# Optimization experiments

Hardware: AMD Instinct MI355X
Metric: run time of the kernel (lower is better)

## Reference

```python
import jax, jax.numpy as jnp
import numpy as np

TRUNCATE = 4.0
SIGMA_MIN, SIGMA_MAX, NUM_STEPS = 0.5, 20.0, 200
RADIUS = int(TRUNCATE * SIGMA_MAX + 0.5)  # 80
KSIZE = 2 * RADIUS + 1                    # 161
B, C, H, W = 64, 3, 512, 512


def setup_inputs() -> dict:
    key = jax.random.key(0)
    k1, k2 = jax.random.split(key)
    x = jax.random.normal(k1, (B, C, H, W), dtype=jnp.float32)
    # geometric sigma schedule, as used in inverse-heat-dissipation models
    blur_sigmas = jnp.exp(
        jnp.linspace(np.log(SIGMA_MIN), np.log(SIGMA_MAX), NUM_STEPS)
    ).astype(jnp.float32)
    fwd_steps = jax.random.randint(k2, (B,), 0, NUM_STEPS, dtype=jnp.int32)
    return {"x": x, "blur_sigmas": blur_sigmas, "fwd_steps": fwd_steps}


def _gaussian_kernels_1d(sigmas, dtype):
    # torchvision formula: normalized exp(-0.5*(t/sigma)^2) on linspace(-half, half, K)
    half = (KSIZE - 1) / 2.0
    t = jnp.linspace(-half, half, KSIZE, dtype=dtype)        # [K]
    pdf = jnp.exp(-0.5 * (t[None, :] / sigmas[:, None]) ** 2)  # [B, K]
    return pdf / pdf.sum(axis=1, keepdims=True)


def reference(x, blur_sigmas, fwd_steps):
    b, c, h, w = x.shape
    sig = blur_sigmas[fwd_steps] + 1e-6                      # [B] per-sample sigma
    k1d = _gaussian_kernels_1d(sig, x.dtype)                 # [B, K]
    kc = jnp.repeat(k1d, c, axis=0)                          # [B*C, K] depthwise

    pad = KSIZE // 2
    xp = jnp.pad(x, ((0, 0), (0, 0), (pad, pad), (pad, pad)), mode="reflect")
    lhs = xp.reshape(1, b * c, h + 2 * pad, w + 2 * pad)

    dn_shape = (1, b * c, 1, 1)  # placeholder rhs shape for dim numbers
    dn = jax.lax.conv_dimension_numbers(lhs.shape, (b * c, 1, KSIZE, 1),
                                        ("NCHW", "OIHW", "NCHW"))
    # vertical pass: [1, BC, H+2p, W+2p] -> [1, BC, H, W+2p]
    y = jax.lax.conv_general_dilated(
        lhs, kc.reshape(b * c, 1, KSIZE, 1), (1, 1), "VALID",
        dimension_numbers=dn, feature_group_count=b * c)
    # horizontal pass: -> [1, BC, H, W]
    y = jax.lax.conv_general_dilated(
        y, kc.reshape(b * c, 1, 1, KSIZE), (1, 1), "VALID",
        dimension_numbers=dn, feature_group_count=b * c)
    return y.reshape(b, c, h, w)
```

## Files before the change

### kernel.cpp

```cpp
#include <hip/hip_runtime.h>
#include <hip/hip_fp16.h>


#define B_   64
#define C_   3
#define H_   512
#define W_   512
#define RMAX 80
#define NW   224
#define WOFF 112
#define RROW1 416
#define IW2   672

typedef float    f32x16 __attribute__((ext_vector_type(16)));
typedef _Float16 f16x8  __attribute__((ext_vector_type(8)));

__device__ __forceinline__ int refl(int g) {
    int a = g < 0 ? -g : g;
    int c = 1022 - a;
    return a < c ? a : c;
}

__device__ __forceinline__ int make_weights(float sigma, float* scr, float* red,
                                            unsigned int* w2v, int tid) {
    const int d = tid - 128;
    float e = 0.f;
    if (d >= -RMAX && d <= RMAX) {
        const float u = (float)d / sigma;
        e = expf(-0.5f * u * u);
    }
    scr[tid] = e;
    red[tid] = e;
    __syncthreads();
    for (int s = 128; s > 0; s >>= 1) {
        if (tid < s) red[tid] += red[tid + s];
        __syncthreads();
    }
    const float inv = 1.0f / red[0];
    int r = (int)ceilf(6.0f * sigma);
    if (r > RMAX) r = RMAX;
    if (r < 1)    r = 1;
    if (tid < NW) {
        const int d0 = tid - 112;
        const float w0 = (d0     >= -r && d0     <= r) ? scr[tid + 16] * inv : 0.f;
        const float w1 = (d0 + 1 >= -r && d0 + 1 <= r) ? scr[tid + 17] * inv : 0.f;
        w2v[tid] = (unsigned int)__half_as_ushort(__float2half(w0)) |
                   ((unsigned int)__half_as_ushort(__float2half(w1)) << 16);
    }
    __syncthreads();
    return r;
}

__global__ __launch_bounds__(256) void k_pass1(const float* __restrict__ x,
                                               const float* __restrict__ sig,
                                               const int* __restrict__ steps,
                                               __half* __restrict__ tmp) {
    __shared__ __align__(16) unsigned short sh[64 * RROW1];
    __shared__ unsigned int w2v[NW];
    const int tid = threadIdx.x;
    int bid = blockIdx.x;
    bid = ((bid & 7) * 384) + (bid >> 3);
    const int bc  = bid >> 4;
    const int rem = bid & 15;
    const int y0  = (rem >> 3) << 8;
    const int x0  = (rem & 7) << 6;
    const int b   = bc / C_;
    const size_t img = (size_t)bc * (H_ * (size_t)W_);

    const float sigma = sig[steps[b]] + 1e-6f;
    float* scr = (float*)sh;
    const int r  = make_weights(sigma, scr, scr + 256, w2v, tid);
    const int rp = (r + 7) & ~7;
    const int ns = (r + rp + 47) >> 4;
    const int Rr = 224 + 16 * ns;
    const int ystart = y0 - rp;

    {
        const int p0 = tid & 15;
        const int x4 = tid >> 4;
        const float* gsrc = x + img + (size_t)(x0 + x4 * 4);
        const int i7 = (2 * p0) & 7;
        for (int pr = p0; 2 * pr < Rr; pr += 16) {
            const int i0  = 2 * pr;
            const int gy0 = refl(ystart + i0);
            const int gy1 = refl(ystart + i0 + 1);
            const float4 va = *(const float4*)(gsrc + (size_t)gy0 * W_);
            const float4 vb = *(const float4*)(gsrc + (size_t)gy1 * W_);
            const float* fa = (const float*)&va;
            const float* fb = (const float*)&vb;
            const int c = i0 >> 3;
            #pragma unroll
            for (int q = 0; q < 4; ++q) {
                const int xq = x4 * 4 + q;
                const int hidx = xq * RROW1 + ((c ^ (xq & 3)) << 3) + i7;
                *(__half2*)(sh + hidx) = __floats2half2_rn(fa[q], fb[q]);
            }
        }
    }
    __syncthreads();

    const int l   = tid & 63;
    const int wv_ = tid >> 6;
    const int m   = l & 31;
    const int g   = l >> 5;
    const int key = m & 3;
    const int ebase = WOFF + 8 * g - rp - m;
    const int cA  = 4 * wv_ + g;
    const int cB  = 4 * (wv_ + 4) + g;
    const unsigned short* shm0 = sh + m * RROW1;
    const unsigned short* shm1 = sh + (32 + m) * RROW1;

    f32x16 a0 = {}, a1 = {}, a2 = {}, a3 = {};
    for (int s = 0; s < ns; ++s) {
        const int e = ebase + 16 * s;
        union { unsigned int u[4]; f16x8 h; } A;
        A.u[0] = w2v[e];     A.u[1] = w2v[e + 2];
        A.u[2] = w2v[e + 4]; A.u[3] = w2v[e + 6];
        const int phA = ((cA + 2 * s) ^ key) << 3;
        const int phB = ((cB + 2 * s) ^ key) << 3;
        const f16x8 b00 = *(const f16x8*)(shm0 + phA);
        const f16x8 b01 = *(const f16x8*)(shm1 + phA);
        const f16x8 b10 = *(const f16x8*)(shm0 + phB);
        const f16x8 b11 = *(const f16x8*)(shm1 + phB);
        a0 = __builtin_amdgcn_mfma_f32_32x32x16_f16(A.h, b00, a0, 0, 0, 0);
        a1 = __builtin_amdgcn_mfma_f32_32x32x16_f16(A.h, b01, a1, 0, 0, 0);
        a2 = __builtin_amdgcn_mfma_f32_32x32x16_f16(A.h, b10, a2, 0, 0, 0);
        a3 = __builtin_amdgcn_mfma_f32_32x32x16_f16(A.h, b11, a3, 0, 0, 0);
    }

    __half* tb0 = tmp + img + (size_t)(y0 + 32 * wv_) * W_ + x0 + m;
    __half* tb1 = tmp + img + (size_t)(y0 + 32 * (wv_ + 4)) * W_ + x0 + m;
    #pragma unroll
    for (int reg = 0; reg < 16; ++reg) {
        const int row = (reg & 3) + 8 * (reg >> 2) + 4 * g;
        tb0[(size_t)row * W_]      = __float2half(a0[reg]);
        tb0[(size_t)row * W_ + 32] = __float2half(a1[reg]);
        tb1[(size_t)row * W_]      = __float2half(a2[reg]);
        tb1[(size_t)row * W_ + 32] = __float2half(a3[reg]);
    }
}

__global__ __launch_bounds__(256) void k_pass2(const __half* __restrict__ tmp,
                                               const float* __restrict__ sig,
                                               const int* __restrict__ steps,
                                               float* __restrict__ out) {
    __shared__ __align__(16) unsigned short sh[32 * IW2];
    __shared__ unsigned int w2v[NW];
    const int tid = threadIdx.x;
    const int bid = blockIdx.x;
    const int bc  = bid >> 4;
    const int y0  = (bid & 15) << 5;
    const int b   = bc / C_;
    const size_t img = (size_t)bc * (H_ * (size_t)W_);

    const float sigma = sig[steps[b]] + 1e-6f;
    float* scr = (float*)sh;
    const int r  = make_weights(sigma, scr, scr + 256, w2v, tid);
    const int rp = (r + 7) & ~7;
    const int ns = (r + rp + 47) >> 4;

    const int row  = tid >> 3;
    const int cq   = tid & 7;
    const int rkey = row & 3;
    {
        const __half* grow = tmp + img + (size_t)(y0 + row) * W_;
        const int cb = rp >> 3;
        for (int k = cq; k < 64; k += 8) {
            const int c = cb + k;
            *(int4*)(sh + row * IW2 + ((c ^ rkey) << 3)) =
                *(const int4*)(grow + k * 8);
        }
    }
    __syncthreads();
    {
        const int nh = 16 * ns - 32;
        const int rbase = row * IW2;
        for (int e = cq; e < nh; e += 8) {
            const int ip = e < rp ? e : e + 512;
            const int gx = ip - rp;
            const int is = refl(gx) + rp;
            const unsigned short v =
                sh[rbase + (((is >> 3) ^ rkey) << 3) + (is & 7)];
            sh[rbase + (((ip >> 3) ^ rkey) << 3) + (ip & 7)] = v;
        }
    }
    __syncthreads();

    const int l   = tid & 63;
    const int wv_ = tid >> 6;
    const int m   = l & 31;
    const int g   = l >> 5;
    const int akey  = m & 3;
    const int ebase = WOFF + 8 * g - rp - m;
    const unsigned short* shm = sh + m * IW2;
    const int c0 = 16 * wv_ + g;

    f32x16 a0 = {}, a1 = {}, a2 = {}, a3 = {};
    for (int s = 0; s < ns; ++s) {
        const int e = ebase + 16 * s;
        union { unsigned int u[4]; f16x8 h; } Wf;
        Wf.u[0] = w2v[e];     Wf.u[1] = w2v[e + 2];
        Wf.u[2] = w2v[e + 4]; Wf.u[3] = w2v[e + 6];
        const int cs = c0 + 2 * s;
        const f16x8 f0 = *(const f16x8*)(shm + (((cs     ) ^ akey) << 3));
        const f16x8 f1 = *(const f16x8*)(shm + (((cs +  4) ^ akey) << 3));
        const f16x8 f2 = *(const f16x8*)(shm + (((cs +  8) ^ akey) << 3));
        const f16x8 f3 = *(const f16x8*)(shm + (((cs + 12) ^ akey) << 3));
        a0 = __builtin_amdgcn_mfma_f32_32x32x16_f16(f0, Wf.h, a0, 0, 0, 0);
        a1 = __builtin_amdgcn_mfma_f32_32x32x16_f16(f1, Wf.h, a1, 0, 0, 0);
        a2 = __builtin_amdgcn_mfma_f32_32x32x16_f16(f2, Wf.h, a2, 0, 0, 0);
        a3 = __builtin_amdgcn_mfma_f32_32x32x16_f16(f3, Wf.h, a3, 0, 0, 0);
    }

    float* ob = out + img + (size_t)y0 * W_ + 128 * wv_ + m;
    #pragma unroll
    for (int reg = 0; reg < 16; ++reg) {
        const int orow = (reg & 3) + 8 * (reg >> 2) + 4 * g;
        float* orp_ = ob + (size_t)orow * W_;
        orp_[0]  = a0[reg];
        orp_[32] = a1[reg];
        orp_[64] = a2[reg];
        orp_[96] = a3[reg];
    }
}

extern "C" void kernel_launch(void* const* d_in, const int* in_sizes, int n_in,
                              void* d_out, int out_size, void* d_ws, size_t ws_size,
                              hipStream_t stream) {
    const float* x     = (const float*)d_in[0];
    const float* sig   = (const float*)d_in[1];
    const int*   steps = (const int*)d_in[2];
    float* out = (float*)d_out;
    __half* tmp = (__half*)d_ws;

    k_pass1<<<B_ * C_ * 16, 256, 0, stream>>>(x, sig, steps, tmp);
    k_pass2<<<B_ * C_ * 16, 256, 0, stream>>>(tmp, sig, steps, out);
}
```

Measured before the change: 398.3 us.

## Fuse vertical and horizontal blur passes into one kernel via LDS intermediate

Merges the two separable-convolution kernels into one. Each block computes the vertical pass for a 32-row strip in eight 64-column chunks and keeps the fp16 result in LDS, then runs the horizontal pass from LDS. This removes the fp16 intermediate round-trip through global memory and one kernel launch. In exchange, each block re-reads the vertical halo rows (up to 2*r extra input rows per 32 output rows), and only two of four waves do MFMA work during the vertical stage, with syncthreads between chunks.

After: 478.5 us. 1.2x slower.

```diff
diff --git a/kernel.cpp b/kernel.cpp
--- a/kernel.cpp
+++ b/kernel.cpp
@@ -9,8 +9,8 @@
 #define RMAX 80
 #define NW   224
 #define WOFF 112
-#define RROW1 416
-#define IW2   672
+#define SB_R 192
+#define IW   704
 
 typedef float    f32x16 __attribute__((ext_vector_type(16)));
 typedef _Float16 f16x8  __attribute__((ext_vector_type(8)));
@@ -51,157 +51,109 @@
     return r;
 }
 
-__global__ __launch_bounds__(256) void k_pass1(const float* __restrict__ x,
-                                               const float* __restrict__ sig,
-                                               const int* __restrict__ steps,
-                                               __half* __restrict__ tmp) {
-    __shared__ __align__(16) unsigned short sh[64 * RROW1];
+__global__ __launch_bounds__(256, 2) void k_fused(const float* __restrict__ x,
+                                                  const float* __restrict__ sig,
+                                                  const int* __restrict__ steps,
+                                                  float* __restrict__ out) {
+    __shared__ __align__(16) unsigned short sbuf[64 * SB_R];
+    __shared__ __align__(16) unsigned short vtmp[32 * IW];
     __shared__ unsigned int w2v[NW];
     const int tid = threadIdx.x;
-    int bid = blockIdx.x;
-    bid = ((bid & 7) * 384) + (bid >> 3);
-    const int bc  = bid >> 4;
-    const int rem = bid & 15;
-    const int y0  = (rem >> 3) << 8;
-    const int x0  = (rem & 7) << 6;
+    const int id  = blockIdx.x;
+    const int xcd = id & 7, idx = id >> 3;
+    const int bc  = xcd * 24 + (idx >> 4);
+    const int y0  = (idx & 15) << 5;
     const int b   = bc / C_;
     const size_t img = (size_t)bc * (H_ * (size_t)W_);
 
     const float sigma = sig[steps[b]] + 1e-6f;
-    float* scr = (float*)sh;
+    float* scr = (float*)sbuf;
     const int r  = make_weights(sigma, scr, scr + 256, w2v, tid);
     const int rp = (r + 7) & ~7;
     const int ns = (r + rp + 47) >> 4;
-    const int Rr = 224 + 16 * ns;
+    const int Rr = 16 * ns;
     const int ystart = y0 - rp;
 
+    const int l  = tid & 63;
+    const int wv = tid >> 6;
+    const int m  = l & 31;
+    const int g  = l >> 5;
+    const int ebase = WOFF + 8 * g - rp - m;
+
+    const int p0 = tid & 15;
+    const int x4 = tid >> 4;
+
+    for (int s = 0; s < 8; ++s) {
+        {
+            const float* gsrc = x + img + (64 * s + x4 * 4);
+            const int i7 = (2 * p0) & 7;
+            for (int pr = p0; 2 * pr < Rr; pr += 16) {
+                const int i0  = 2 * pr;
+                const int gy0 = refl(ystart + i0);
+                const int gy1 = refl(ystart + i0 + 1);
+                const float4 va = *(const float4*)(gsrc + (size_t)gy0 * W_);
+                const float4 vb = *(const float4*)(gsrc + (size_t)gy1 * W_);
+                const float* fa = (const float*)&va;
+                const float* fb = (const float*)&vb;
+                const int c = i0 >> 3;
+                #pragma unroll
+                for (int q = 0; q < 4; ++q) {
+                    const int xq = x4 * 4 + q;
+                    *(__half2*)(sbuf + xq * SB_R + ((c ^ (xq & 3)) << 3) + i7) =
+                        __floats2half2_rn(fa[q], fb[q]);
+                }
+            }
+        }
+        __syncthreads();
+        if (wv < 2) {
+            const unsigned short* arow = sbuf + (32 * wv + m) * SB_R;
+            const int akey = m & 3;
+            f32x16 acc = {};
+            for (int sk = 0; sk < ns; ++sk) {
+                const int e = ebase + 16 * sk;
+                union { unsigned int u[4]; f16x8 h; } Wf;
+                Wf.u[0] = w2v[e];     Wf.u[1] = w2v[e + 2];
+                Wf.u[2] = w2v[e + 4]; Wf.u[3] = w2v[e + 6];
+                const f16x8 af = *(const f16x8*)(arow + (((2 * sk + g) ^ akey) << 3));
+                acc = __builtin_amdgcn_mfma_f32_32x32x16_f16(af, Wf.h, acc, 0, 0, 0);
+            }
+            const int ybase = m * IW;
+            const int key   = m & 7;
+            #pragma unroll
+            for (int t = 0; t < 8; ++t) {
+                const int off4 = 4 * g + 2 * (t & 1);
+                const int c2   = (rp >> 3) + 8 * s + 4 * wv + (t >> 1);
+                *(__half2*)(vtmp + ybase + ((c2 ^ key) << 3) + off4) =
+                    __floats2half2_rn(acc[2 * t], acc[2 * t + 1]);
+            }
+        }
+        __syncthreads();
+    }
+
     {
-        const int p0 = tid & 15;
-        const int x4 = tid >> 4;
-        const float* gsrc = x + img + (size_t)(x0 + x4 * 4);
-        const int i7 = (2 * p0) & 7;
-        for (int pr = p0; 2 * pr < Rr; pr += 16) {
-            const int i0  = 2 * pr;
-            const int gy0 = refl(ystart + i0);
-            const int gy1 = refl(ystart + i0 + 1);
-            const float4 va = *(const float4*)(gsrc + (size_t)gy0 * W_);
-            const float4 vb = *(const float4*)(gsrc + (size_t)gy1 * W_);
-            const float* fa = (const float*)&va;
-            const float* fb = (const float*)&vb;
-            const int c = i0 >> 3;
-            #pragma unroll
-            for (int q = 0; q < 4; ++q) {
-                const int xq = x4 * 4 + q;
-                const int hidx = xq * RROW1 + ((c ^ (xq & 3)) << 3) + i7;
-                *(__half2*)(sh + hidx) = __floats2half2_rn(fa[q], fb[q]);
-            }
+        const int nh   = 16 * ns - 32;
+        const int row  = tid >> 3, cq = tid & 7;
+        const int rbase = row * IW, key = row & 7;
+        for (int e = cq; e < nh; e += 8) {
+            const int ip = e < rp ? e : e + 512;
+            const int is = refl(ip - rp) + rp;
+            const unsigned short v =
+                vtmp[rbase + (((is >> 3) ^ key) << 3) + (is & 7)];
+            vtmp[rbase + (((ip >> 3) ^ key) << 3) + (ip & 7)] = v;
         }
     }
     __syncthreads();
 
-    const int l   = tid & 63;
-    const int wv_ = tid >> 6;
-    const int m   = l & 31;
-    const int g   = l >> 5;
-    const int key = m & 3;
-    const int ebase = WOFF + 8 * g - rp - m;
-    const int cA  = 4 * wv_ + g;
-    const int cB  = 4 * (wv_ + 4) + g;
-    const unsigned short* shm0 = sh + m * RROW1;
-    const unsigned short* shm1 = sh + (32 + m) * RROW1;
-
+    const unsigned short* shm = vtmp + m * IW;
+    const int akey = m & 7;
+    const int c0   = 16 * wv + g;
     f32x16 a0 = {}, a1 = {}, a2 = {}, a3 = {};
-    for (int s = 0; s < ns; ++s) {
-        const int e = ebase + 16 * s;
-        union { unsigned int u[4]; f16x8 h; } A;
-        A.u[0] = w2v[e];     A.u[1] = w2v[e + 2];
-        A.u[2] = w2v[e + 4]; A.u[3] = w2v[e + 6];
-        const int phA = ((cA + 2 * s) ^ key) << 3;
-        const int phB = ((cB + 2 * s) ^ key) << 3;
-        const f16x8 b00 = *(const f16x8*)(shm0 + phA);
-        const f16x8 b01 = *(const f16x8*)(shm1 + phA);
-        const f16x8 b10 = *(const f16x8*)(shm0 + phB);
-        const f16x8 b11 = *(const f16x8*)(shm1 + phB);
-        a0 = __builtin_amdgcn_mfma_f32_32x32x16_f16(A.h, b00, a0, 0, 0, 0);
-        a1 = __builtin_amdgcn_mfma_f32_32x32x16_f16(A.h, b01, a1, 0, 0, 0);
-        a2 = __builtin_amdgcn_mfma_f32_32x32x16_f16(A.h, b10, a2, 0, 0, 0);
-        a3 = __builtin_amdgcn_mfma_f32_32x32x16_f16(A.h, b11, a3, 0, 0, 0);
-    }
-
-    __half* tb0 = tmp + img + (size_t)(y0 + 32 * wv_) * W_ + x0 + m;
-    __half* tb1 = tmp + img + (size_t)(y0 + 32 * (wv_ + 4)) * W_ + x0 + m;
-    #pragma unroll
-    for (int reg = 0; reg < 16; ++reg) {
-        const int row = (reg & 3) + 8 * (reg >> 2) + 4 * g;
-        tb0[(size_t)row * W_]      = __float2half(a0[reg]);
-        tb0[(size_t)row * W_ + 32] = __float2half(a1[reg]);
-        tb1[(size_t)row * W_]      = __float2half(a2[reg]);
-        tb1[(size_t)row * W_ + 32] = __float2half(a3[reg]);
-    }
-}
-
-__global__ __launch_bounds__(256) void k_pass2(const __half* __restrict__ tmp,
-                                               const float* __restrict__ sig,
-                                               const int* __restrict__ steps,
-                                               float* __restrict__ out) {
-    __shared__ __align__(16) unsigned short sh[32 * IW2];
-    __shared__ unsigned int w2v[NW];
-    const int tid = threadIdx.x;
-    const int bid = blockIdx.x;
-    const int bc  = bid >> 4;
-    const int y0  = (bid & 15) << 5;
-    const int b   = bc / C_;
-    const size_t img = (size_t)bc * (H_ * (size_t)W_);
-
-    const float sigma = sig[steps[b]] + 1e-6f;
-    float* scr = (float*)sh;
-    const int r  = make_weights(sigma, scr, scr + 256, w2v, tid);
-    const int rp = (r + 7) & ~7;
-    const int ns = (r + rp + 47) >> 4;
-
-    const int row  = tid >> 3;
-    const int cq   = tid & 7;
-    const int rkey = row & 3;
-    {
-        const __half* grow = tmp + img + (size_t)(y0 + row) * W_;
-        const int cb = rp >> 3;
-        for (int k = cq; k < 64; k += 8) {
-            const int c = cb + k;
-            *(int4*)(sh + row * IW2 + ((c ^ rkey) << 3)) =
-                *(const int4*)(grow + k * 8);
-        }
-    }
-    __syncthreads();
-    {
-        const int nh = 16 * ns - 32;
-        const int rbase = row * IW2;
-        for (int e = cq; e < nh; e += 8) {
-            const int ip = e < rp ? e : e + 512;
-            const int gx = ip - rp;
-            const int is = refl(gx) + rp;
-            const unsigned short v =
-                sh[rbase + (((is >> 3) ^ rkey) << 3) + (is & 7)];
-            sh[rbase + (((ip >> 3) ^ rkey) << 3) + (ip & 7)] = v;
-        }
-    }
-    __syncthreads();
-
-    const int l   = tid & 63;
-    const int wv_ = tid >> 6;
-    const int m   = l & 31;
-    const int g   = l >> 5;
-    const int akey  = m & 3;
-    const int ebase = WOFF + 8 * g - rp - m;
-    const unsigned short* shm = sh + m * IW2;
-    const int c0 = 16 * wv_ + g;
-
-    f32x16 a0 = {}, a1 = {}, a2 = {}, a3 = {};
-    for (int s = 0; s < ns; ++s) {
-        const int e = ebase + 16 * s;
+    for (int sk = 0; sk < ns; ++sk) {
+        const int e = ebase + 16 * sk;
         union { unsigned int u[4]; f16x8 h; } Wf;
         Wf.u[0] = w2v[e];     Wf.u[1] = w2v[e + 2];
         Wf.u[2] = w2v[e + 4]; Wf.u[3] = w2v[e + 6];
-        const int cs = c0 + 2 * s;
+        const int cs = c0 + 2 * sk;
         const f16x8 f0 = *(const f16x8*)(shm + (((cs     ) ^ akey) << 3));
         const f16x8 f1 = *(const f16x8*)(shm + (((cs +  4) ^ akey) << 3));
         const f16x8 f2 = *(const f16x8*)(shm + (((cs +  8) ^ akey) << 3));
@@ -212,7 +164,7 @@
         a3 = __builtin_amdgcn_mfma_f32_32x32x16_f16(f3, Wf.h, a3, 0, 0, 0);
     }
 
-    float* ob = out + img + (size_t)y0 * W_ + 128 * wv_ + m;
+    float* ob = out + img + (size_t)y0 * W_ + 128 * wv + m;
     #pragma unroll
     for (int reg = 0; reg < 16; ++reg) {
         const int orow = (reg & 3) + 8 * (reg >> 2) + 4 * g;
@@ -231,8 +183,7 @@
     const float* sig   = (const float*)d_in[1];
     const int*   steps = (const int*)d_in[2];
     float* out = (float*)d_out;
-    __half* tmp = (__half*)d_ws;
+    (void)d_ws; (void)ws_size;
 
-    k_pass1<<<B_ * C_ * 16, 256, 0, stream>>>(x, sig, steps, tmp);
-    k_pass2<<<B_ * C_ * 16, 256, 0, stream>>>(tmp, sig, steps, out);
+    k_fused<<<B_ * C_ * 16, 256, 0, stream>>>(x, sig, steps, out);
 }
```
